# Kernel tuning notes

Measured on AMD Instinct MI355X. Metric: run time of the kernel, lower is better.

Reference implementation:

```python
import jax, jax.numpy as jnp
import numpy as np

B, S, D_MODEL = 1, 2048, 4096
N_HEADS, N_KV_HEADS = 32, 8
HEAD_DIM = D_MODEL // N_HEADS  # 128
N_REP = N_HEADS // N_KV_HEADS  # 4
ROPE_THETA = 500000.0
NEG_INF = -1e9


def setup_inputs() -> dict:
    key = jax.random.key(0)
    ks = jax.random.split(key, 6)
    std = 0.02 * (2 * 32) ** (-0.5)
    x = jax.random.normal(ks[0], (B, S, D_MODEL), dtype=jnp.float32)
    wq = jax.random.normal(ks[1], (N_HEADS * HEAD_DIM, D_MODEL), dtype=jnp.float32) * std
    wk = jax.random.normal(ks[2], (N_KV_HEADS * HEAD_DIM, D_MODEL), dtype=jnp.float32) * std
    wv = jax.random.normal(ks[3], (N_KV_HEADS * HEAD_DIM, D_MODEL), dtype=jnp.float32) * std
    wo = jax.random.normal(ks[4], (D_MODEL, N_HEADS * HEAD_DIM), dtype=jnp.float32) * std
    cache_k = jnp.zeros((B, S, N_KV_HEADS, HEAD_DIM), dtype=jnp.float32)
    cache_v = jnp.zeros((B, S, N_KV_HEADS, HEAD_DIM), dtype=jnp.float32)
    # RoPE tables: freqs_cis[t, j] = exp(i * t * theta^(-2j/head_dim)), j < head_dim/2
    inv_freq = 1.0 / (ROPE_THETA ** (jnp.arange(0, HEAD_DIM, 2, dtype=jnp.float32) / HEAD_DIM))
    t = jnp.arange(S, dtype=jnp.float32)
    ang = jnp.outer(t, inv_freq)  # [S, HEAD_DIM/2]
    freqs_cos = jnp.cos(ang)
    freqs_sin = jnp.sin(ang)
    # causal additive mask [1, 1, S, S]
    mask = jnp.triu(jnp.full((S, S), NEG_INF, dtype=jnp.float32), k=1)[None, None]
    return {"x": x, "wq": wq, "wk": wk, "wv": wv, "wo": wo,
            "cache_k": cache_k, "cache_v": cache_v,
            "freqs_cos": freqs_cos, "freqs_sin": freqs_sin,
            "mask": mask, "start_pos": 0}


def _apply_rope(x, cos, sin):
    # x: [B, S, H, D]; cos/sin: [S, D/2]; pairs (x[2j], x[2j+1]) form complex numbers
    b, s, h, d = x.shape
    x2 = x.astype(jnp.float32).reshape(b, s, h, d // 2, 2)
    xr, xi = x2[..., 0], x2[..., 1]
    c = cos[None, :, None, :]
    sn = sin[None, :, None, :]
    out_r = xr * c - xi * sn
    out_i = xr * sn + xi * c
    return jnp.stack([out_r, out_i], axis=-1).reshape(b, s, h, d)


def reference(x, wq, wk, wv, wo, cache_k, cache_v, freqs_cos, freqs_sin, mask, start_pos):
    bsz, seq_len, _ = x.shape
    xq = (x @ wq.T).reshape(bsz, seq_len, N_HEADS, HEAD_DIM)
    xk = (x @ wk.T).reshape(bsz, seq_len, N_KV_HEADS, HEAD_DIM)
    xv = (x @ wv.T).reshape(bsz, seq_len, N_KV_HEADS, HEAD_DIM)
    xq = _apply_rope(xq, freqs_cos, freqs_sin)
    xk = _apply_rope(xk, freqs_cos, freqs_sin)
    # KV-cache update then read back the valid prefix
    cache_k = jax.lax.dynamic_update_slice(cache_k, xk, (0, start_pos, 0, 0))
    cache_v = jax.lax.dynamic_update_slice(cache_v, xv, (0, start_pos, 0, 0))
    keys = cache_k[:, : start_pos + seq_len]      # [B, K, KVH, D]
    values = cache_v[:, : start_pos + seq_len]
    # repeat_kv: expand kv heads to match query heads
    keys = jnp.repeat(keys, N_REP, axis=2)        # [B, K, H, D]
    values = jnp.repeat(values, N_REP, axis=2)
    q = xq.transpose(0, 2, 1, 3)                  # [B, H, S, D]
    k = keys.transpose(0, 2, 1, 3)                # [B, H, K, D]
    v = values.transpose(0, 2, 1, 3)
    scores = jnp.einsum('bhqd,bhkd->bhqk', q, k) / jnp.float32(np.sqrt(HEAD_DIM))
    scores = scores + mask
    probs = jax.nn.softmax(scores.astype(jnp.float32), axis=-1).astype(q.dtype)
    out = jnp.einsum('bhqk,bhkd->bhqd', probs, v)           # [B, H, S, D]
    out = out.transpose(0, 2, 1, 3).reshape(bsz, seq_len, -1)
    return out @ wo.T
```

## Files before the change

kernel.cpp:

```cpp
#include <hip/hip_runtime.h>
#include <cstdint>
#include <cstddef>

typedef __attribute__((ext_vector_type(8))) short  short8;
typedef __attribute__((ext_vector_type(4))) float  floatx4;
typedef __attribute__((ext_vector_type(4))) unsigned short ushort4v;

__device__ __forceinline__ unsigned short f2b(float f) {
  unsigned u = __builtin_bit_cast(unsigned, f);
  u = u + 0x7fffu + ((u >> 16) & 1u);
  return (unsigned short)(u >> 16);
}

__device__ __forceinline__ void gld_lds16(const void* g, void* l) {
  __builtin_amdgcn_global_load_lds(
      (const __attribute__((address_space(1))) unsigned int*)g,
      (__attribute__((address_space(3))) unsigned int*)l,
      16, 0, 0);
}

__device__ __forceinline__ short8 ds_read_b128v(const unsigned short* p) {
  short8 r;
  asm volatile("ds_read_b128 %0, %1"
               : "=v"(r)
               : "v"((const __attribute__((address_space(3))) unsigned short*)p));
  return r;
}
__device__ __forceinline__ void ds_write_b16v(unsigned short* p, unsigned short v) {
  asm volatile("ds_write_b16 %0, %1"
               :: "v"((__attribute__((address_space(3))) unsigned short*)p),
                  "v"((unsigned)v)
               : "memory");
}

#define LGKM_FENCE(N)                                        \
  do {                                                       \
    asm volatile("s_waitcnt lgkmcnt(" #N ")" ::: "memory");  \
    __builtin_amdgcn_sched_barrier(0);                       \
  } while (0)
#define LGKM0_FENCE() LGKM_FENCE(0)

__global__ void __launch_bounds__(256) f2b_kernel(const float* __restrict__ in,
                                                  unsigned short* __restrict__ out,
                                                  int n4) {
  int i = blockIdx.x * 256 + threadIdx.x;
  if (i >= n4) return;
  floatx4 v = ((const floatx4*)in)[i];
  ushort4v o;
  o[0] = f2b(v[0]); o[1] = f2b(v[1]); o[2] = f2b(v[2]); o[3] = f2b(v[3]);
  ((ushort4v*)out)[i] = o;
}

template <int MODE, int BN>
__global__ void __launch_bounds__(512, 2)
gemm256(const unsigned short* __restrict__ A,
        const unsigned short* __restrict__ B,
        float* __restrict__ Cf,
        unsigned short* __restrict__ Cb,
        int K, int N,
        const float* __restrict__ fc,
        const float* __restrict__ fs) {
  constexpr int BM = 256, BK = 64;
  constexpr int NF  = BN / 64;
  constexpr int WNC = BN / 4;
  constexpr int NB  = BN / 64;

  __shared__ __align__(16) unsigned short As[2][BM * BK];
  __shared__ __align__(16) unsigned short Bs[2][BN * BK];

  const int tid  = threadIdx.x;
  const int wave = tid >> 6, lane = tid & 63;
  const int quad = lane >> 4, l15 = lane & 15;
  const int wr = wave >> 2, wc = wave & 3;

  int flat = blockIdx.y * 8 + blockIdx.x;
  const int cpx = (int)(gridDim.x * gridDim.y) >> 3;
  flat = (flat & 7) * cpx + (flat >> 3);
  const int m0 = (flat & 7) * BM;
  const int n0 = (flat >> 3) * BN;

  const int srow = lane >> 3;
  const int soct = (lane & 7) ^ srow;
  const unsigned short* pa[4];
  const unsigned short* pb[NB];
#pragma unroll
  for (int i = 0; i < 4; ++i)
    pa[i] = A + (size_t)(m0 + wave * 32 + i * 8 + srow) * K + soct * 8;
#pragma unroll
  for (int i = 0; i < NB; ++i)
    pb[i] = B + (size_t)(n0 + wave * (BN / 8) + i * 8 + srow) * K + soct * 8;

  const int xr = l15 & 7;
  int aoff[2], boff[2];
#pragma unroll
  for (int ks = 0; ks < 2; ++ks) {
    const int sl = ((ks * 4 + quad) ^ xr) * 8;
    aoff[ks] = (wr * 128 + l15) * 64 + sl;
    boff[ks] = (wc * WNC + l15) * 64 + sl;
  }

  floatx4 acc[8][NF] = {};
  const int NT = K >> 6;

#pragma unroll
  for (int i = 0; i < 4; ++i)
    gld_lds16(pa[i], &As[0][(wave * 32 + i * 8) * 64]);
#pragma unroll
  for (int i = 0; i < NB; ++i)
    gld_lds16(pb[i], &Bs[0][(wave * (BN / 8) + i * 8) * 64]);
  asm volatile("s_waitcnt vmcnt(0)" ::: "memory");
  __builtin_amdgcn_s_barrier();
  __builtin_amdgcn_sched_barrier(0);

  int t = 0, kt = 0;

#define TILE_STEP(BUF)                                                         \
  do {                                                                         \
    short8 bfr[NF][2], afr[2][2];                                              \
    _Pragma("unroll") for (int n = 0; n < NF; ++n)                             \
      _Pragma("unroll") for (int ks = 0; ks < 2; ++ks)                         \
        bfr[n][ks] = ds_read_b128v(&Bs[BUF][boff[ks] + n * 1024]);             \
    _Pragma("unroll") for (int mm = 0; mm < 2; ++mm)                           \
      _Pragma("unroll") for (int ks = 0; ks < 2; ++ks)                         \
        afr[mm][ks] = ds_read_b128v(&As[BUF][aoff[ks] + mm * 1024]);           \
    if (t + 1 < NT) {                                                          \
      const int kn = kt + 64;                                                  \
      _Pragma("unroll") for (int i = 0; i < 4; ++i)                            \
        gld_lds16(pa[i] + kn, &As[1 - (BUF)][(wave * 32 + i * 8) * 64]);       \
      _Pragma("unroll") for (int i = 0; i < NB; ++i)                           \
        gld_lds16(pb[i] + kn, &Bs[1 - (BUF)][(wave * (BN / 8) + i * 8) * 64]); \
    }                                                                          \
    __builtin_amdgcn_s_barrier();                                              \
    LGKM0_FENCE();                                                             \
    __builtin_amdgcn_s_setprio(1);                                             \
    _Pragma("unroll") for (int mm = 0; mm < 2; ++mm)                           \
      _Pragma("unroll") for (int n = 0; n < NF; ++n)                           \
        _Pragma("unroll") for (int ks = 0; ks < 2; ++ks)                       \
          acc[mm][n] = __builtin_amdgcn_mfma_f32_16x16x32_bf16(                \
              afr[mm][ks], bfr[n][ks], acc[mm][n], 0, 0, 0);                   \
    __builtin_amdgcn_s_setprio(0);                                             \
    __builtin_amdgcn_s_barrier();                                              \
    _Pragma("unroll") for (int p = 1; p < 4; ++p) {                            \
      short8 a2[2][2];                                                         \
      _Pragma("unroll") for (int mm = 0; mm < 2; ++mm)                         \
        _Pragma("unroll") for (int ks = 0; ks < 2; ++ks)                       \
          a2[mm][ks] =                                                         \
              ds_read_b128v(&As[BUF][aoff[ks] + (p * 2 + mm) * 1024]);         \
      __builtin_amdgcn_s_barrier();                                            \
      LGKM0_FENCE();                                                           \
      __builtin_amdgcn_s_setprio(1);                                           \
      _Pragma("unroll") for (int mm = 0; mm < 2; ++mm)                         \
        _Pragma("unroll") for (int n = 0; n < NF; ++n)                         \
          _Pragma("unroll") for (int ks = 0; ks < 2; ++ks)                     \
            acc[p * 2 + mm][n] = __builtin_amdgcn_mfma_f32_16x16x32_bf16(      \
                a2[mm][ks], bfr[n][ks], acc[p * 2 + mm][n], 0, 0, 0);          \
      __builtin_amdgcn_s_setprio(0);                                           \
      if (p == 3) asm volatile("s_waitcnt vmcnt(0)" ::: "memory");             \
      __builtin_amdgcn_s_barrier();                                            \
    }                                                                          \
    __builtin_amdgcn_sched_barrier(0);                                         \
    kt += 64;                                                                  \
    ++t;                                                                       \
  } while (0)

  while (t < NT) {
    TILE_STEP(0);
    TILE_STEP(1);
  }
#undef TILE_STEP

#pragma unroll
  for (int mi = 0; mi < 8; ++mi) {
#pragma unroll
    for (int n = 0; n < NF; ++n) {
      const int colb = n0 + wc * WNC + n * 16;
      const int col  = colb + l15;
      const bool rope = (MODE == 2) && (colb < 5120);
      const int pp = (col & 127) >> 1;
      const float sgn = (l15 & 1) ? 1.f : -1.f;
#pragma unroll
      for (int r = 0; r < 4; ++r) {
        const int row = m0 + wr * 128 + mi * 16 + quad * 4 + r;
        float v = acc[mi][n][r];
        if (rope) {
          const float partner = __shfl_xor(v, 1);
          const float c  = fc[row * 64 + pp];
          const float sn = fs[row * 64 + pp];
          v = v * c + partner * sn * sgn;
        }
        if (MODE == 1) Cf[(size_t)row * N + col] = v;
        else           Cb[(size_t)row * N + col] = f2b(v);
      }
    }
  }
}

__global__ void __launch_bounds__(256) transpose_bf16(const unsigned short* __restrict__ in,
                                                      unsigned short* __restrict__ out,
                                                      int R, int C, int in_stride) {
  __shared__ __align__(16) unsigned short tile[64][72];
  const int br = blockIdx.y * 64;
  const int bc = blockIdx.x * 64;
  const int tid = threadIdx.x;
  const int lr = tid >> 3;
  const int lc = (tid & 7) * 8;
#pragma unroll
  for (int it = 0; it < 2; ++it) {
    const int r = it * 32 + lr;
    *(short8*)&tile[r][lc] = *(const short8*)(in + (size_t)(br + r) * in_stride + bc + lc);
  }
  __syncthreads();
#pragma unroll
  for (int it = 0; it < 2; ++it) {
    const int c = it * 32 + lr;
    short8 v;
#pragma unroll
    for (int j = 0; j < 8; ++j) v[j] = (short)tile[lc + j][c];
    *(short8*)(out + (size_t)(bc + c) * R + br + lc) = v;
  }
}

#define SL2E 0.1275500406721347f

__global__ void __launch_bounds__(256) flash_attn(const unsigned short* __restrict__ Q,
                                                  const unsigned short* __restrict__ Kp,
                                                  const unsigned short* __restrict__ Vt,
                                                  unsigned short* __restrict__ O) {
  constexpr int QS = 6144;
  const int bx  = blockIdx.x;
  const int h   = blockIdx.y;
  const int kvh = h >> 2;
  const int tid = threadIdx.x;
  const int wave = tid >> 6, lane = tid & 63;
  const int quad = lane >> 4, l15 = lane & 15;
  const int xr8 = l15 & 7;

  __shared__ __align__(16) unsigned short Ks[2][8192];
  __shared__ __align__(16) unsigned short Vs[2][8192];
  __shared__ __align__(16) unsigned short Ps[4][16 * 88];
  unsigned short* Pw = Ps[wave];

  const unsigned short* kp4[4];
  const unsigned short* vp4[4];
#pragma unroll
  for (int ii = 0; ii < 4; ++ii) {
    const int k0   = wave * 16 + ii * 4;
    const int krow = k0 + (lane >> 4);
    const int goct = (lane & 15) ^ (krow & 7);
    kp4[ii] = Kp + kvh * 128 + (size_t)krow * QS + goct * 8;
    const int d0   = wave * 32 + ii * 8;
    const int drow = d0 + (lane >> 3);
    const int voct = (lane & 7) ^ ((lane >> 3) & 7);
    vp4[ii] = Vt + (size_t)(kvh * 128 + drow) * 2048 + voct * 8;
  }

  for (int seg = 0; seg < 2; ++seg) {
    const int qt  = seg ? (31 - bx) : bx;
    const int qra = qt * 64 + wave * 16;
    const int n   = qt + 1;

    short8 aq[4];
#pragma unroll
    for (int ks = 0; ks < 4; ++ks)
      aq[ks] = *(const short8*)(Q + (size_t)(qra + l15) * QS + h * 128 + ks * 32 + quad * 8);

    floatx4 oacc[8] = {};
    float mrow[4], lrow[4];
#pragma unroll
    for (int r = 0; r < 4; ++r) { mrow[r] = -1e30f; lrow[r] = 0.f; }

#pragma unroll
    for (int ii = 0; ii < 4; ++ii) {
      gld_lds16(kp4[ii], &Ks[0][wave * 2048 + ii * 512]);
      gld_lds16(vp4[ii], &Vs[0][wave * 2048 + ii * 512]);
    }

    for (int j = 0; j < n; ++j) {
      asm volatile("s_waitcnt vmcnt(0)" ::: "memory");
      __builtin_amdgcn_s_barrier();
      __builtin_amdgcn_sched_barrier(0);
      const unsigned short* kb = Ks[j & 1];
      const unsigned short* vb = Vs[j & 1];
      const int c0 = j * 64;

      floatx4 sacc[4] = {};
      {
        short8 bkA[4], bkB[4];
#pragma unroll
        for (int tn = 0; tn < 4; ++tn)
          bkA[tn] = ds_read_b128v(&kb[(tn * 16 + l15) * 128 + ((quad ^ xr8) * 8)]);
#pragma unroll
        for (int tn = 0; tn < 4; ++tn)
          bkB[tn] = ds_read_b128v(&kb[(tn * 16 + l15) * 128 + (((4 + quad) ^ xr8) * 8)]);
        LGKM_FENCE(4);
        __builtin_amdgcn_s_setprio(1);
#pragma unroll
        for (int tn = 0; tn < 4; ++tn)
          sacc[tn] = __builtin_amdgcn_mfma_f32_16x16x32_bf16(aq[0], bkA[tn], sacc[tn], 0, 0, 0);
        __builtin_amdgcn_s_setprio(0);
#pragma unroll
        for (int tn = 0; tn < 4; ++tn)
          bkA[tn] = ds_read_b128v(&kb[(tn * 16 + l15) * 128 + (((8 + quad) ^ xr8) * 8)]);
        LGKM_FENCE(4);
        __builtin_amdgcn_s_setprio(1);
#pragma unroll
        for (int tn = 0; tn < 4; ++tn)
          sacc[tn] = __builtin_amdgcn_mfma_f32_16x16x32_bf16(aq[1], bkB[tn], sacc[tn], 0, 0, 0);
        __builtin_amdgcn_s_setprio(0);
#pragma unroll
        for (int tn = 0; tn < 4; ++tn)
          bkB[tn] = ds_read_b128v(&kb[(tn * 16 + l15) * 128 + (((12 + quad) ^ xr8) * 8)]);
        LGKM_FENCE(4);
        __builtin_amdgcn_s_setprio(1);
#pragma unroll
        for (int tn = 0; tn < 4; ++tn)
          sacc[tn] = __builtin_amdgcn_mfma_f32_16x16x32_bf16(aq[2], bkA[tn], sacc[tn], 0, 0, 0);
        __builtin_amdgcn_s_setprio(0);
        LGKM_FENCE(0);
        __builtin_amdgcn_s_setprio(1);
#pragma unroll
        for (int tn = 0; tn < 4; ++tn)
          sacc[tn] = __builtin_amdgcn_mfma_f32_16x16x32_bf16(aq[3], bkB[tn], sacc[tn], 0, 0, 0);
        __builtin_amdgcn_s_setprio(0);
      }

      const bool needmask = (c0 + 63 > qra);
#pragma unroll
      for (int r = 0; r < 4; ++r) {
        const int rowg = qra + quad * 4 + r;
        float t0 = sacc[0][r] * SL2E, t1 = sacc[1][r] * SL2E;
        float t2 = sacc[2][r] * SL2E, t3 = sacc[3][r] * SL2E;
        if (needmask) {
          t0 = (c0 +  0 + l15 <= rowg) ? t0 : -1e30f;
          t1 = (c0 + 16 + l15 <= rowg) ? t1 : -1e30f;
          t2 = (c0 + 32 + l15 <= rowg) ? t2 : -1e30f;
          t3 = (c0 + 48 + l15 <= rowg) ? t3 : -1e30f;
        }
        float mx = fmaxf(fmaxf(t0, t1), fmaxf(t2, t3));
#pragma unroll
        for (int off = 1; off < 16; off <<= 1)
          mx = fmaxf(mx, __shfl_xor(mx, off, 16));
        const float mold = mrow[r];
        const float mn   = fmaxf(mold, mx);
        const float alpha = exp2f(mold - mn);
        float p0 = exp2f(t0 - mn), p1 = exp2f(t1 - mn);
        float p2 = exp2f(t2 - mn), p3 = exp2f(t3 - mn);
        sacc[0][r] = p0; sacc[1][r] = p1; sacc[2][r] = p2; sacc[3][r] = p3;
        float lsum = (p0 + p1) + (p2 + p3);
#pragma unroll
        for (int off = 1; off < 16; off <<= 1)
          lsum += __shfl_xor(lsum, off, 16);
        mrow[r] = mn;
        lrow[r] = lrow[r] * alpha + lsum;
#pragma unroll
        for (int tn = 0; tn < 8; ++tn) oacc[tn][r] *= alpha;
      }

      if (j + 1 < n) {
        const int cc = (j + 1) * 64;
        const int nb = (j + 1) & 1;
#pragma unroll
        for (int ii = 0; ii < 4; ++ii) {
          gld_lds16(kp4[ii] + (size_t)cc * QS, &Ks[nb][wave * 2048 + ii * 512]);
          gld_lds16(vp4[ii] + cc, &Vs[nb][wave * 2048 + ii * 512]);
        }
      }

#pragma unroll
      for (int tn = 0; tn < 4; ++tn)
#pragma unroll
        for (int r = 0; r < 4; ++r)
          ds_write_b16v(&Pw[(quad * 4 + r) * 88 + tn * 16 + l15], f2b(sacc[tn][r]));
      short8 ap0 = ds_read_b128v(&Pw[l15 * 88 + quad * 8]);
      short8 ap1 = ds_read_b128v(&Pw[l15 * 88 + 32 + quad * 8]);
      short8 bv0[8], bv1[8];
#pragma unroll
      for (int tn = 0; tn < 8; ++tn)
        bv0[tn] = ds_read_b128v(&vb[(tn * 16 + l15) * 64 + ((quad ^ xr8) * 8)]);
#pragma unroll
      for (int tn = 0; tn < 8; ++tn)
        bv1[tn] = ds_read_b128v(&vb[(tn * 16 + l15) * 64 + (((4 + quad) ^ xr8) * 8)]);
      LGKM_FENCE(8);
      __builtin_amdgcn_s_setprio(1);
#pragma unroll
      for (int tn = 0; tn < 8; ++tn)
        oacc[tn] = __builtin_amdgcn_mfma_f32_16x16x32_bf16(ap0, bv0[tn], oacc[tn], 0, 0, 0);
      __builtin_amdgcn_s_setprio(0);
      LGKM_FENCE(0);
      __builtin_amdgcn_s_setprio(1);
#pragma unroll
      for (int tn = 0; tn < 8; ++tn)
        oacc[tn] = __builtin_amdgcn_mfma_f32_16x16x32_bf16(ap1, bv1[tn], oacc[tn], 0, 0, 0);
      __builtin_amdgcn_s_setprio(0);
    }

#pragma unroll
    for (int r = 0; r < 4; ++r) {
      const float inv = 1.f / lrow[r];
      const int rowg = qra + quad * 4 + r;
#pragma unroll
      for (int tn = 0; tn < 8; ++tn)
        O[(size_t)rowg * 4096 + h * 128 + tn * 16 + l15] = f2b(oacc[tn][r] * inv);
    }
    __syncthreads();
  }
}

extern "C" void kernel_launch(void* const* d_in, const int* in_sizes, int n_in,
                              void* d_out, int out_size, void* d_ws, size_t ws_size,
                              hipStream_t stream) {
  const float* x  = (const float*)d_in[0];
  const float* wq = (const float*)d_in[1];
  const float* wk = (const float*)d_in[2];
  const float* wv = (const float*)d_in[3];
  const float* wo = (const float*)d_in[4];
  const float* fc = (const float*)d_in[7];
  const float* fs = (const float*)d_in[8];
  float* out = (float*)d_out;

  char* ws = (char*)d_ws;
  unsigned short* xb    = (unsigned short*)(ws + 0);
  unsigned short* wqkvb = (unsigned short*)(ws + 16777216);
  unsigned short* wob   = (unsigned short*)(ws + 67108864);
  unsigned short* qkv   = (unsigned short*)(ws + 100663296);
  unsigned short* vt    = (unsigned short*)(ws + 125829120);
  unsigned short* ob    = (unsigned short*)(ws + 130023424);
  unsigned short* wkb = wqkvb + (size_t)4096 * 4096;
  unsigned short* wvb = wkb + (size_t)1024 * 4096;

  f2b_kernel<<<8192,  256, 0, stream>>>(x,  xb,    2097152);
  f2b_kernel<<<16384, 256, 0, stream>>>(wq, wqkvb, 4194304);
  f2b_kernel<<<4096,  256, 0, stream>>>(wk, wkb,   1048576);
  f2b_kernel<<<4096,  256, 0, stream>>>(wv, wvb,   1048576);
  f2b_kernel<<<16384, 256, 0, stream>>>(wo, wob,   4194304);

  gemm256<2, 192><<<dim3(8, 32), 512, 0, stream>>>(xb, wqkvb, nullptr, qkv,
                                                   4096, 6144, fc, fs);

  transpose_bf16<<<dim3(16, 32), 256, 0, stream>>>(qkv + 5120, vt, 2048, 1024, 6144);

  flash_attn<<<dim3(16, 32), 256, 0, stream>>>(qkv, qkv + 4096, vt, ob);

  gemm256<1, 128><<<dim3(8, 32), 512, 0, stream>>>(ob, wob, out, nullptr,
                                                   4096, 4096, nullptr, nullptr);
}
```

Before: 549.3 us.

## Software-pipeline A-fragment LDS reads and drop per-group barriers in GEMM tile step

```diff
diff --git a/kernel.cpp b/kernel.cpp
--- a/kernel.cpp
+++ b/kernel.cpp
@@ -50,6 +50,18 @@
   o[0] = f2b(v[0]); o[1] = f2b(v[1]); o[2] = f2b(v[2]); o[3] = f2b(v[3]);
   ((ushort4v*)out)[i] = o;
 }
+
+#define ISSUE_A(BUF, dst, g)                                                   \
+    _Pragma("unroll") for (int mm = 0; mm < 2; ++mm)                           \
+      _Pragma("unroll") for (int ks = 0; ks < 2; ++ks)                         \
+        dst[mm][ks] = ds_read_b128v(&As[BUF][aoff[ks] + ((g) * 2 + mm) * 1024]);
+
+#define MFMA_G(src, g)                                                         \
+    _Pragma("unroll") for (int mm = 0; mm < 2; ++mm)                           \
+      _Pragma("unroll") for (int n = 0; n < NF; ++n)                           \
+        _Pragma("unroll") for (int ks = 0; ks < 2; ++ks)                       \
+          acc[(g) * 2 + mm][n] = __builtin_amdgcn_mfma_f32_16x16x32_bf16(      \
+              src[mm][ks], bfr[n][ks], acc[(g) * 2 + mm][n], 0, 0, 0);
 
 template <int MODE, int BN>
 __global__ void __launch_bounds__(512, 2)
@@ -116,13 +128,12 @@
 
 #define TILE_STEP(BUF)                                                         \
   do {                                                                         \
-    short8 bfr[NF][2], afr[2][2];                                              \
+    short8 bfr[NF][2], a0[2][2], a1[2][2], a2[2][2], a3[2][2];                 \
     _Pragma("unroll") for (int n = 0; n < NF; ++n)                             \
       _Pragma("unroll") for (int ks = 0; ks < 2; ++ks)                         \
         bfr[n][ks] = ds_read_b128v(&Bs[BUF][boff[ks] + n * 1024]);             \
-    _Pragma("unroll") for (int mm = 0; mm < 2; ++mm)                           \
-      _Pragma("unroll") for (int ks = 0; ks < 2; ++ks)                         \
-        afr[mm][ks] = ds_read_b128v(&As[BUF][aoff[ks] + mm * 1024]);           \
+    ISSUE_A(BUF, a0, 0);                                                       \
+    ISSUE_A(BUF, a1, 1);                                                       \
     if (t + 1 < NT) {                                                          \
       const int kn = kt + 64;                                                  \
       _Pragma("unroll") for (int i = 0; i < 4; ++i)                            \
@@ -130,34 +141,26 @@
       _Pragma("unroll") for (int i = 0; i < NB; ++i)                           \
         gld_lds16(pb[i] + kn, &Bs[1 - (BUF)][(wave * (BN / 8) + i * 8) * 64]); \
     }                                                                          \
-    __builtin_amdgcn_s_barrier();                                              \
-    LGKM0_FENCE();                                                             \
+    LGKM_FENCE(4);        \
     __builtin_amdgcn_s_setprio(1);                                             \
-    _Pragma("unroll") for (int mm = 0; mm < 2; ++mm)                           \
-      _Pragma("unroll") for (int n = 0; n < NF; ++n)                           \
-        _Pragma("unroll") for (int ks = 0; ks < 2; ++ks)                       \
-          acc[mm][n] = __builtin_amdgcn_mfma_f32_16x16x32_bf16(                \
-              afr[mm][ks], bfr[n][ks], acc[mm][n], 0, 0, 0);                   \
+    MFMA_G(a0, 0);                                                             \
     __builtin_amdgcn_s_setprio(0);                                             \
-    __builtin_amdgcn_s_barrier();                                              \
-    _Pragma("unroll") for (int p = 1; p < 4; ++p) {                            \
-      short8 a2[2][2];                                                         \
-      _Pragma("unroll") for (int mm = 0; mm < 2; ++mm)                         \
-        _Pragma("unroll") for (int ks = 0; ks < 2; ++ks)                       \
-          a2[mm][ks] =                                                         \
-              ds_read_b128v(&As[BUF][aoff[ks] + (p * 2 + mm) * 1024]);         \
-      __builtin_amdgcn_s_barrier();                                            \
-      LGKM0_FENCE();                                                           \
-      __builtin_amdgcn_s_setprio(1);                                           \
-      _Pragma("unroll") for (int mm = 0; mm < 2; ++mm)                         \
-        _Pragma("unroll") for (int n = 0; n < NF; ++n)                         \
-          _Pragma("unroll") for (int ks = 0; ks < 2; ++ks)                     \
-            acc[p * 2 + mm][n] = __builtin_amdgcn_mfma_f32_16x16x32_bf16(      \
-                a2[mm][ks], bfr[n][ks], acc[p * 2 + mm][n], 0, 0, 0);          \
-      __builtin_amdgcn_s_setprio(0);                                           \
-      if (p == 3) asm volatile("s_waitcnt vmcnt(0)" ::: "memory");             \
-      __builtin_amdgcn_s_barrier();                                            \
-    }                                                                          \
+    ISSUE_A(BUF, a2, 2);                                                       \
+    LGKM_FENCE(4);                               \
+    __builtin_amdgcn_s_setprio(1);                                             \
+    MFMA_G(a1, 1);                                                             \
+    __builtin_amdgcn_s_setprio(0);                                             \
+    ISSUE_A(BUF, a3, 3);                                                       \
+    LGKM_FENCE(4);                               \
+    __builtin_amdgcn_s_setprio(1);                                             \
+    MFMA_G(a2, 2);                                                             \
+    __builtin_amdgcn_s_setprio(0);                                             \
+    LGKM_FENCE(0);                                            \
+    __builtin_amdgcn_s_setprio(1);                                             \
+    MFMA_G(a3, 3);                                                             \
+    __builtin_amdgcn_s_setprio(0);                                             \
+    asm volatile("s_waitcnt vmcnt(0)" ::: "memory");   \
+    __builtin_amdgcn_s_barrier();     \
     __builtin_amdgcn_sched_barrier(0);                                         \
     kt += 64;                                                                  \
     ++t;                                                                       \
```

Result: faster. 538.5 us (-2.0%).
